# Kernel optimization log

Hardware: AMD Instinct MI355X
Metric: run time of the kernel (lower is better)

The kernel has to match this reference:

```python
import jax, jax.numpy as jnp
import numpy as np

SEQ, B, IN, H, OUT = 600, 4096, 6, 30, 61


def setup_inputs() -> dict:
    key = jax.random.key(0)
    ks = jax.random.split(key, 9)
    s_ih = 1.0 / np.sqrt(H)
    return {
        "X": jax.random.normal(ks[0], (SEQ, B, IN), dtype=jnp.float32),
        "W_ih": jax.random.uniform(ks[1], (4 * H, IN), jnp.float32, -s_ih, s_ih),
        "W_hh": jax.random.uniform(ks[2], (4 * H, H), jnp.float32, -s_ih, s_ih),
        "b_ih": jax.random.uniform(ks[3], (4 * H,), jnp.float32, -s_ih, s_ih),
        "b_hh": jax.random.uniform(ks[4], (4 * H,), jnp.float32, -s_ih, s_ih),
        "W1": jax.random.uniform(ks[5], (H, H), jnp.float32, -s_ih, s_ih),
        "b1": jax.random.uniform(ks[6], (H,), jnp.float32, -s_ih, s_ih),
        "W2": jax.random.uniform(ks[7], (OUT, H), jnp.float32, -s_ih, s_ih),
        "b2": jax.random.uniform(ks[8], (OUT,), jnp.float32, -s_ih, s_ih),
        "batch_size": B,
    }


def _lstm_last_h(X, W_ih, W_hh, b_ih, b_hh):
    # Precompute input projections for all timesteps: [T, B, 4H]
    xg = jnp.einsum("tbi,gi->tbg", X, W_ih) + b_ih + b_hh
    h0 = jnp.zeros((X.shape[1], W_hh.shape[1]), X.dtype)
    c0 = jnp.zeros_like(h0)

    def step(carry, xg_t):
        h, c = carry
        g = xg_t + h @ W_hh.T  # [B, 4H]
        i, f, gg, o = jnp.split(g, 4, axis=-1)  # PyTorch gate order i,f,g,o
        c = jax.nn.sigmoid(f) * c + jax.nn.sigmoid(i) * jnp.tanh(gg)
        h = jax.nn.sigmoid(o) * jnp.tanh(c)
        return (h, c), None

    (h, _), _ = jax.lax.scan(step, (h0, c0), xg)
    return h  # out[-1, :, :]


def reference(X, W_ih, W_hh, b_ih, b_hh, W1, b1, W2, b2, batch_size):
    h = _lstm_last_h(X, W_ih, W_hh, b_ih, b_hh)
    out = h @ W1.T + b1  # fc1
    # dropout(p=0.6) is identity in eval mode
    out = out @ W2.T + b2  # fc2
    return out  # [B, 61]
```

## Files before the change

### kernel.cpp

```cpp
#include <hip/hip_runtime.h>


#define SEQ   600
#define BATCH 4096
#define INP   6
#define HID   30
#define NOUT  61
#define WPB   2

typedef __fp16 f16;
typedef f16  f16x2 __attribute__((ext_vector_type(2)));
typedef float f32x2 __attribute__((ext_vector_type(2)));

__device__ __forceinline__ float rcp_(float x)  { return __builtin_amdgcn_rcpf(x); }
__device__ __forceinline__ float exp2_(float x) { return __builtin_amdgcn_exp2f(x); }
__device__ __forceinline__ f16x2 as_h2(unsigned v) {
    union { unsigned u; f16x2 h; } c; c.u = v; return c.h;
}
#define LOG2E  1.4426950408889634f
#define LOG2E2 2.8853900817779268f

extern "C" __global__ void __launch_bounds__(64 * WPB, 4)
lstm_fused6(const float* __restrict__ X,   const float* __restrict__ Wih,
            const float* __restrict__ Whh, const float* __restrict__ bih,
            const float* __restrict__ bhh, const float* __restrict__ W1,
            const float* __restrict__ b1,  const float* __restrict__ W2,
            const float* __restrict__ b2,  float* __restrict__ out)
{
    __shared__ __align__(16) f16 h_sh[WPB][32];
    __shared__ float o1_sh[WPB][32];

    const int tid  = threadIdx.x;
    const int lane = tid & 63;
    const int u    = lane & 31;
    const int half = lane >> 5;
    const int e    = tid >> 6;
    const int b    = blockIdx.x * WPB + e;
    const int uu   = (u < HID) ? u : (HID - 1);
    const bool act = (u < HID);

    if (lane < 32) h_sh[e][lane] = (f16)0.f;

    const int rowA = (half ? 2 : 0) * HID + uu;
    const int rowB = (half ? 3 : 1) * HID + uu;

    const float* ra = Whh + rowA * HID;
    const float* rb = Whh + rowB * HID;
    f16x2 wA[15], wB[15];
    #pragma unroll
    for (int j = 0; j < 15; ++j) {
        wA[j] = f16x2{(f16)ra[2 * j], (f16)ra[2 * j + 1]};
        wB[j] = f16x2{(f16)rb[2 * j], (f16)rb[2 * j + 1]};
    }
    const float* sa = Wih + rowA * INP;
    const float* sb = Wih + rowB * INP;
    f16x2 xwA[3], xwB[3];
    #pragma unroll
    for (int j = 0; j < 3; ++j) {
        xwA[j] = f16x2{(f16)sa[2 * j], (f16)sa[2 * j + 1]};
        xwB[j] = f16x2{(f16)sb[2 * j], (f16)sb[2 * j + 1]};
    }
    float bA = 0.f, bB = 0.f;
    if (act) {
        bA = bih[rowA] + bhh[rowA];
        bB = bih[rowB] + bhh[rowB];
    }

    #pragma unroll
    for (int j = 0; j < 15; ++j) asm("" : "+v"(wA[j]), "+v"(wB[j]));
    #pragma unroll
    for (int j = 0; j < 3; ++j)  asm("" : "+v"(xwA[j]), "+v"(xwB[j]));
    asm("" : "+v"(bA), "+v"(bB));

    const float mA = half ? -LOG2E2 : -LOG2E;
    const float sA = half ? 2.0f : 1.0f;
    const float cA = half ? -1.0f : 0.0f;

    float c = 0.f, h = 0.f;

    f32x2 xc0, xc1, xc2, xn0, xn1, xn2;
    {
        const f32x2* p = (const f32x2*)(X + (size_t)b * INP);
        xc0 = p[0]; xc1 = p[1]; xc2 = p[2];
    }
    asm volatile("s_waitcnt lgkmcnt(0)" ::: "memory");

    const uint4* hq = (const uint4*)(&h_sh[e][0]);

    for (int t = 0; t < SEQ; ++t) {
        const int tn = (t + 1 < SEQ) ? (t + 1) : (SEQ - 1);
        const f32x2* p = (const f32x2*)(X + ((size_t)tn * BATCH + b) * INP);
        xn0 = p[0]; xn1 = p[1]; xn2 = p[2];

        const uint4 Hq0 = hq[0], Hq1 = hq[1], Hq2 = hq[2], Hq3 = hq[3];
        const f16x2 hp[16] = {
            as_h2(Hq0.x), as_h2(Hq0.y), as_h2(Hq0.z), as_h2(Hq0.w),
            as_h2(Hq1.x), as_h2(Hq1.y), as_h2(Hq1.z), as_h2(Hq1.w),
            as_h2(Hq2.x), as_h2(Hq2.y), as_h2(Hq2.z), as_h2(Hq2.w),
            as_h2(Hq3.x), as_h2(Hq3.y), as_h2(Hq3.z), as_h2(Hq3.w)
        };

        float aAe = bA, aAo = 0.f, aBe = bB, aBo = 0.f;
        #define DOT(J, E) do {                                            \
            aA##E = __builtin_amdgcn_fdot2(wA[J], hp[J], aA##E, false);   \
            aB##E = __builtin_amdgcn_fdot2(wB[J], hp[J], aB##E, false);   \
        } while (0)
        DOT(0, e);  DOT(1, o);  DOT(2, e);  DOT(3, o);
        DOT(4, e);  DOT(5, o);  DOT(6, e);  DOT(7, o);
        DOT(8, e);  DOT(9, o);  DOT(10, e); DOT(11, o);
        DOT(12, e); DOT(13, o); DOT(14, e);
        #undef DOT
        const f16x2 xh0 = __builtin_amdgcn_cvt_pkrtz(xc0.x, xc0.y);
        const f16x2 xh1 = __builtin_amdgcn_cvt_pkrtz(xc1.x, xc1.y);
        const f16x2 xh2 = __builtin_amdgcn_cvt_pkrtz(xc2.x, xc2.y);
        aAo = __builtin_amdgcn_fdot2(xwA[0], xh0, aAo, false);
        aBo = __builtin_amdgcn_fdot2(xwB[0], xh0, aBo, false);
        aAe = __builtin_amdgcn_fdot2(xwA[1], xh1, aAe, false);
        aBe = __builtin_amdgcn_fdot2(xwB[1], xh1, aBe, false);
        aAo = __builtin_amdgcn_fdot2(xwA[2], xh2, aAo, false);
        aBo = __builtin_amdgcn_fdot2(xwB[2], xh2, aBo, false);

        const float aA = aAe + aAo;
        const float aB = aBe + aBo;

        const float nA = fmaf(sA, rcp_(1.0f + exp2_(mA * aA)), cA);
        const float nB = rcp_(1.0f + exp2_(-LOG2E * aB));

        const float vA = __shfl_xor(nA, 32);
        const float vB = __shfl_xor(nB, 32);

        const float F = half ? vB : nB;
        const float O = half ? nB : vB;
        c = fmaf(F, c, nA * vA);
        const float tc = 1.0f - 2.0f * rcp_(exp2_(LOG2E2 * c) + 1.0f);
        h = O * tc;

        if (lane < HID) h_sh[e][lane] = (f16)h;
        asm volatile("s_waitcnt lgkmcnt(0)" ::: "memory");

        xc0 = xn0; xc1 = xn1; xc2 = xn2;
    }

    if (lane < HID) {
        float a1 = b1[lane];
        const float* w1r = W1 + lane * HID;
        #pragma unroll
        for (int k = 0; k < HID; ++k) a1 = fmaf(w1r[k], (float)h_sh[e][k], a1);
        o1_sh[e][lane] = a1;
    }
    asm volatile("s_waitcnt lgkmcnt(0)" ::: "memory");

    if (lane < NOUT) {
        float a2 = b2[lane];
        const float* w2r = W2 + lane * HID;
        #pragma unroll
        for (int k = 0; k < HID; ++k) a2 = fmaf(w2r[k], o1_sh[e][k], a2);
        out[(size_t)b * NOUT + lane] = a2;
    }
}

extern "C" void kernel_launch(void* const* d_in, const int* in_sizes, int n_in,
                              void* d_out, int out_size, void* d_ws, size_t ws_size,
                              hipStream_t stream) {
    const float* X   = (const float*)d_in[0];
    const float* Wih = (const float*)d_in[1];
    const float* Whh = (const float*)d_in[2];
    const float* bih = (const float*)d_in[3];
    const float* bhh = (const float*)d_in[4];
    const float* W1  = (const float*)d_in[5];
    const float* b1  = (const float*)d_in[6];
    const float* W2  = (const float*)d_in[7];
    const float* b2  = (const float*)d_in[8];
    float* out = (float*)d_out;

    dim3 grid(BATCH / WPB);
    dim3 block(64 * WPB);
    hipLaunchKernelGGL(lstm_fused6, grid, block, 0, stream,
                       X, Wih, Whh, bih, bhh, W1, b1, W2, b2, out);
}
```

Baseline: 386.7 us.

## Process two batch elements per wavefront with interleaved recurrent steps

Each 64-lane wavefront now advances two independent batch sequences instead of one. Every timestep runs both recurrences back to back, so their dependency chains can overlap and hide latency. X is loaded as three float4 per step covering both elements, which replaces smaller per-element loads, and each element keeps its own shared-memory h row. The cost is that the grid has half as many wavefronts, and the launch bound drops to 2 waves, which allows more registers per wave but may cut the occupancy available to hide latency.

```diff
diff --git a/kernel.cpp b/kernel.cpp
--- a/kernel.cpp
+++ b/kernel.cpp
@@ -6,11 +6,9 @@
 #define INP   6
 #define HID   30
 #define NOUT  61
-#define WPB   2
 
 typedef __fp16 f16;
 typedef f16  f16x2 __attribute__((ext_vector_type(2)));
-typedef float f32x2 __attribute__((ext_vector_type(2)));
 
 __device__ __forceinline__ float rcp_(float x)  { return __builtin_amdgcn_rcpf(x); }
 __device__ __forceinline__ float exp2_(float x) { return __builtin_amdgcn_exp2f(x); }
@@ -20,26 +18,74 @@
 #define LOG2E  1.4426950408889634f
 #define LOG2E2 2.8853900817779268f
 
-extern "C" __global__ void __launch_bounds__(64 * WPB, 4)
-lstm_fused6(const float* __restrict__ X,   const float* __restrict__ Wih,
+__device__ __forceinline__ void step_elem(
+    const f16x2* __restrict__ wA, const f16x2* __restrict__ wB,
+    const f16x2* __restrict__ xwA, const f16x2* __restrict__ xwB,
+    float bA, float bB, const uint4* __restrict__ hq,
+    f16x2 xh0, f16x2 xh1, f16x2 xh2,
+    float mA, float sA, float cA, int half, int lane,
+    float& c, f16* __restrict__ hrow)
+{
+    const uint4 Q0 = hq[0], Q1 = hq[1], Q2 = hq[2], Q3 = hq[3];
+    const f16x2 hp[16] = {
+        as_h2(Q0.x), as_h2(Q0.y), as_h2(Q0.z), as_h2(Q0.w),
+        as_h2(Q1.x), as_h2(Q1.y), as_h2(Q1.z), as_h2(Q1.w),
+        as_h2(Q2.x), as_h2(Q2.y), as_h2(Q2.z), as_h2(Q2.w),
+        as_h2(Q3.x), as_h2(Q3.y), as_h2(Q3.z), as_h2(Q3.w)
+    };
+
+    float aAe = bA, aAo = 0.f, aBe = bB, aBo = 0.f;
+    #define DOT(J, E) do {                                            \
+        aA##E = __builtin_amdgcn_fdot2(wA[J], hp[J], aA##E, false);   \
+        aB##E = __builtin_amdgcn_fdot2(wB[J], hp[J], aB##E, false);   \
+    } while (0)
+    DOT(0, e);  DOT(1, o);  DOT(2, e);  DOT(3, o);
+    DOT(4, e);  DOT(5, o);  DOT(6, e);  DOT(7, o);
+    DOT(8, e);  DOT(9, o);  DOT(10, e); DOT(11, o);
+    DOT(12, e); DOT(13, o); DOT(14, e);
+    #undef DOT
+    aAo = __builtin_amdgcn_fdot2(xwA[0], xh0, aAo, false);
+    aBo = __builtin_amdgcn_fdot2(xwB[0], xh0, aBo, false);
+    aAe = __builtin_amdgcn_fdot2(xwA[1], xh1, aAe, false);
+    aBe = __builtin_amdgcn_fdot2(xwB[1], xh1, aBe, false);
+    aAo = __builtin_amdgcn_fdot2(xwA[2], xh2, aAo, false);
+    aBo = __builtin_amdgcn_fdot2(xwB[2], xh2, aBo, false);
+
+    const float aA = aAe + aAo;
+    const float aB = aBe + aBo;
+
+    const float nA = fmaf(sA, rcp_(1.0f + exp2_(mA * aA)), cA);
+    const float nB = rcp_(1.0f + exp2_(-LOG2E * aB));
+
+    const float vA = __shfl_xor(nA, 32);
+    const float vB = __shfl_xor(nB, 32);
+
+    const float F = half ? vB : nB;
+    const float O = half ? nB : vB;
+    c = fmaf(F, c, nA * vA);
+    const float tc = 1.0f - 2.0f * rcp_(exp2_(LOG2E2 * c) + 1.0f);
+    const float h = O * tc;
+
+    if (lane < HID) hrow[lane] = (f16)h;
+}
+
+extern "C" __global__ void __launch_bounds__(64, 2)
+lstm_fused8(const float* __restrict__ X,   const float* __restrict__ Wih,
             const float* __restrict__ Whh, const float* __restrict__ bih,
             const float* __restrict__ bhh, const float* __restrict__ W1,
             const float* __restrict__ b1,  const float* __restrict__ W2,
             const float* __restrict__ b2,  float* __restrict__ out)
 {
-    __shared__ __align__(16) f16 h_sh[WPB][32];
-    __shared__ float o1_sh[WPB][32];
-
-    const int tid  = threadIdx.x;
-    const int lane = tid & 63;
+    __shared__ __align__(16) f16 h_sh[2][32];
+    __shared__ float o1_sh[2][32];
+
+    const int lane = threadIdx.x;
     const int u    = lane & 31;
     const int half = lane >> 5;
-    const int e    = tid >> 6;
-    const int b    = blockIdx.x * WPB + e;
     const int uu   = (u < HID) ? u : (HID - 1);
-    const bool act = (u < HID);
-
-    if (lane < 32) h_sh[e][lane] = (f16)0.f;
+    const int b0   = blockIdx.x * 2;
+
+    if (lane < 32) { h_sh[0][lane] = (f16)0.f; h_sh[1][lane] = (f16)0.f; }
 
     const int rowA = (half ? 2 : 0) * HID + uu;
     const int rowB = (half ? 3 : 1) * HID + uu;
@@ -60,11 +106,8 @@
         xwA[j] = f16x2{(f16)sa[2 * j], (f16)sa[2 * j + 1]};
         xwB[j] = f16x2{(f16)sb[2 * j], (f16)sb[2 * j + 1]};
     }
-    float bA = 0.f, bB = 0.f;
-    if (act) {
-        bA = bih[rowA] + bhh[rowA];
-        bB = bih[rowB] + bhh[rowB];
-    }
+    float bA = bih[rowA] + bhh[rowA];
+    float bB = bih[rowB] + bhh[rowB];
 
     #pragma unroll
     for (int j = 0; j < 15; ++j) asm("" : "+v"(wA[j]), "+v"(wB[j]));
@@ -76,86 +119,67 @@
     const float sA = half ? 2.0f : 1.0f;
     const float cA = half ? -1.0f : 0.0f;
 
-    float c = 0.f, h = 0.f;
-
-    f32x2 xc0, xc1, xc2, xn0, xn1, xn2;
+    float c0s = 0.f, c1s = 0.f;
+
+    float4 xq0, xq1, xq2;
     {
-        const f32x2* p = (const f32x2*)(X + (size_t)b * INP);
-        xc0 = p[0]; xc1 = p[1]; xc2 = p[2];
-    }
+        const float4* q = (const float4*)(X + (size_t)b0 * INP);
+        xq0 = q[0]; xq1 = q[1]; xq2 = q[2];
+    }
+    const float* pn = X + (size_t)BATCH * INP + (size_t)b0 * INP;
+
     asm volatile("s_waitcnt lgkmcnt(0)" ::: "memory");
 
-    const uint4* hq = (const uint4*)(&h_sh[e][0]);
-
-    for (int t = 0; t < SEQ; ++t) {
-        const int tn = (t + 1 < SEQ) ? (t + 1) : (SEQ - 1);
-        const f32x2* p = (const f32x2*)(X + ((size_t)tn * BATCH + b) * INP);
-        xn0 = p[0]; xn1 = p[1]; xn2 = p[2];
-
-        const uint4 Hq0 = hq[0], Hq1 = hq[1], Hq2 = hq[2], Hq3 = hq[3];
-        const f16x2 hp[16] = {
-            as_h2(Hq0.x), as_h2(Hq0.y), as_h2(Hq0.z), as_h2(Hq0.w),
-            as_h2(Hq1.x), as_h2(Hq1.y), as_h2(Hq1.z), as_h2(Hq1.w),
-            as_h2(Hq2.x), as_h2(Hq2.y), as_h2(Hq2.z), as_h2(Hq2.w),
-            as_h2(Hq3.x), as_h2(Hq3.y), as_h2(Hq3.z), as_h2(Hq3.w)
-        };
-
-        float aAe = bA, aAo = 0.f, aBe = bB, aBo = 0.f;
-        #define DOT(J, E) do {                                            \
-            aA##E = __builtin_amdgcn_fdot2(wA[J], hp[J], aA##E, false);   \
-            aB##E = __builtin_amdgcn_fdot2(wB[J], hp[J], aB##E, false);   \
-        } while (0)
-        DOT(0, e);  DOT(1, o);  DOT(2, e);  DOT(3, o);
-        DOT(4, e);  DOT(5, o);  DOT(6, e);  DOT(7, o);
-        DOT(8, e);  DOT(9, o);  DOT(10, e); DOT(11, o);
-        DOT(12, e); DOT(13, o); DOT(14, e);
-        #undef DOT
-        const f16x2 xh0 = __builtin_amdgcn_cvt_pkrtz(xc0.x, xc0.y);
-        const f16x2 xh1 = __builtin_amdgcn_cvt_pkrtz(xc1.x, xc1.y);
-        const f16x2 xh2 = __builtin_amdgcn_cvt_pkrtz(xc2.x, xc2.y);
-        aAo = __builtin_amdgcn_fdot2(xwA[0], xh0, aAo, false);
-        aBo = __builtin_amdgcn_fdot2(xwB[0], xh0, aBo, false);
-        aAe = __builtin_amdgcn_fdot2(xwA[1], xh1, aAe, false);
-        aBe = __builtin_amdgcn_fdot2(xwB[1], xh1, aBe, false);
-        aAo = __builtin_amdgcn_fdot2(xwA[2], xh2, aAo, false);
-        aBo = __builtin_amdgcn_fdot2(xwB[2], xh2, aBo, false);
-
-        const float aA = aAe + aAo;
-        const float aB = aBe + aBo;
-
-        const float nA = fmaf(sA, rcp_(1.0f + exp2_(mA * aA)), cA);
-        const float nB = rcp_(1.0f + exp2_(-LOG2E * aB));
-
-        const float vA = __shfl_xor(nA, 32);
-        const float vB = __shfl_xor(nB, 32);
-
-        const float F = half ? vB : nB;
-        const float O = half ? nB : vB;
-        c = fmaf(F, c, nA * vA);
-        const float tc = 1.0f - 2.0f * rcp_(exp2_(LOG2E2 * c) + 1.0f);
-        h = O * tc;
-
-        if (lane < HID) h_sh[e][lane] = (f16)h;
-        asm volatile("s_waitcnt lgkmcnt(0)" ::: "memory");
-
-        xc0 = xn0; xc1 = xn1; xc2 = xn2;
-    }
+    const uint4* hq0 = (const uint4*)(&h_sh[0][0]);
+    const uint4* hq1 = (const uint4*)(&h_sh[1][0]);
+
+    #define DO_STEP() do {                                                      \
+        const f16x2 xa0 = __builtin_amdgcn_cvt_pkrtz(xq0.x, xq0.y);             \
+        const f16x2 xa1 = __builtin_amdgcn_cvt_pkrtz(xq0.z, xq0.w);             \
+        const f16x2 xa2 = __builtin_amdgcn_cvt_pkrtz(xq1.x, xq1.y);             \
+        const f16x2 xb0 = __builtin_amdgcn_cvt_pkrtz(xq1.z, xq1.w);             \
+        const f16x2 xb1 = __builtin_amdgcn_cvt_pkrtz(xq2.x, xq2.y);             \
+        const f16x2 xb2 = __builtin_amdgcn_cvt_pkrtz(xq2.z, xq2.w);             \
+        step_elem(wA, wB, xwA, xwB, bA, bB, hq0, xa0, xa1, xa2,                 \
+                  mA, sA, cA, half, lane, c0s, &h_sh[0][0]);                    \
+        step_elem(wA, wB, xwA, xwB, bA, bB, hq1, xb0, xb1, xb2,                 \
+                  mA, sA, cA, half, lane, c1s, &h_sh[1][0]);                    \
+        asm volatile("s_waitcnt lgkmcnt(0)" ::: "memory");                      \
+    } while (0)
+
+    for (int t = 0; t < SEQ - 1; ++t) {
+        const float4* q = (const float4*)pn;
+        const float4 yq0 = q[0], yq1 = q[1], yq2 = q[2];
+        pn += (size_t)BATCH * INP;
+
+        DO_STEP();
+
+        xq0 = yq0; xq1 = yq1; xq2 = yq2;
+    }
+    DO_STEP();
+    #undef DO_STEP
 
     if (lane < HID) {
-        float a1 = b1[lane];
         const float* w1r = W1 + lane * HID;
         #pragma unroll
-        for (int k = 0; k < HID; ++k) a1 = fmaf(w1r[k], (float)h_sh[e][k], a1);
-        o1_sh[e][lane] = a1;
+        for (int e = 0; e < 2; ++e) {
+            float a1 = b1[lane];
+            #pragma unroll
+            for (int k = 0; k < HID; ++k) a1 = fmaf(w1r[k], (float)h_sh[e][k], a1);
+            o1_sh[e][lane] = a1;
+        }
     }
     asm volatile("s_waitcnt lgkmcnt(0)" ::: "memory");
 
     if (lane < NOUT) {
-        float a2 = b2[lane];
         const float* w2r = W2 + lane * HID;
         #pragma unroll
-        for (int k = 0; k < HID; ++k) a2 = fmaf(w2r[k], o1_sh[e][k], a2);
-        out[(size_t)b * NOUT + lane] = a2;
+        for (int e = 0; e < 2; ++e) {
+            float a2 = b2[lane];
+            #pragma unroll
+            for (int k = 0; k < HID; ++k) a2 = fmaf(w2r[k], o1_sh[e][k], a2);
+            out[(size_t)(b0 + e) * NOUT + lane] = a2;
+        }
     }
 }
 
@@ -173,8 +197,8 @@
     const float* b2  = (const float*)d_in[8];
     float* out = (float*)d_out;
 
-    dim3 grid(BATCH / WPB);
-    dim3 block(64 * WPB);
-    hipLaunchKernelGGL(lstm_fused6, grid, block, 0, stream,
+    dim3 grid(BATCH / 2);
+    dim3 block(64);
+    hipLaunchKernelGGL(lstm_fused8, grid, block, 0, stream,
                        X, Wih, Whh, bih, bhh, W1, b1, W2, b2, out);
 }
```

After: 476.4 us. +23.2%, slower.
